# Optimization experiments

Measured on AMD Instinct MI355X. Metric: run time of the kernel, lower is better.

The kernel has to match this reference:

```python
import jax, jax.numpy as jnp
import numpy as np

PH, PW = 7, 7  # pooled_height, pooled_width
B, H, W, C, R = 4, 64, 64, 256, 128


def setup_inputs() -> dict:
    key = jax.random.key(0)
    k1, k2, k3 = jax.random.split(key, 3)
    feature_map = jax.random.normal(k1, (B, H, W, C), dtype=jnp.float32)
    # ROIs: (y_min, x_min, y_max, x_max) relative coords; sized so every
    # region has >= PH rows / PW cols (avoids empty-bin -inf edge case).
    start = jax.random.uniform(k2, (B, R, 2), minval=0.0, maxval=0.4)
    extent = jax.random.uniform(k3, (B, R, 2), minval=0.3, maxval=0.55)
    rois = jnp.concatenate([start, start + extent], axis=-1).astype(jnp.float32)
    return {"feature_map": feature_map, "rois": rois}


def _pool_image(fm, rois_img):
    # fm: (H, W, C); rois_img: (R, 4)
    h, w, _ = fm.shape
    # tf.cast(float->int32) truncates; coords are non-negative so == floor
    h0 = jnp.floor(h * rois_img[:, 0]).astype(jnp.int32)
    w0 = jnp.floor(w * rois_img[:, 1]).astype(jnp.int32)
    h1 = jnp.floor(h * rois_img[:, 2]).astype(jnp.int32)
    w1 = jnp.floor(w * rois_img[:, 3]).astype(jnp.int32)
    rh, rw = h1 - h0, w1 - w0
    hstep = jnp.maximum(rh // PH, 1)  # guard: assumes region >= pooled grid
    wstep = jnp.maximum(rw // PW, 1)

    # Map each absolute row/col to its pooled bin (or PH/PW = "outside").
    rel_h = jnp.arange(h)[None, :] - h0[:, None]            # (R, H)
    bin_h = jnp.clip(rel_h // hstep[:, None], 0, PH - 1)     # last bin extends to region end
    row_id = jnp.where((rel_h >= 0) & (rel_h < rh[:, None]), bin_h, PH)
    rel_w = jnp.arange(w)[None, :] - w0[:, None]            # (R, W)
    bin_w = jnp.clip(rel_w // wstep[:, None], 0, PW - 1)
    col_id = jnp.where((rel_w >= 0) & (rel_w < rw[:, None]), bin_w, PW)

    # Stage 1: segment-max over rows -> (R, PH, W, C)
    seg_rows = jax.vmap(
        lambda ids: jax.ops.segment_max(fm, ids, num_segments=PH + 1)
    )(row_id)[:, :PH]

    # Stage 2: segment-max over cols -> (R, PH, PW, C)
    def col_pool(t, ids):  # t: (PH, W, C)
        tt = jnp.swapaxes(t, 0, 1)  # (W, PH, C)
        s = jax.ops.segment_max(tt, ids, num_segments=PW + 1)[:PW]
        return jnp.swapaxes(s, 0, 1)  # (PH, PW, C)

    return jax.vmap(col_pool)(seg_rows, col_id)


def reference(feature_map, rois):
    # (B, R, PH, PW, C)
    return jax.vmap(_pool_image)(feature_map, rois)
```

## Files before the change

### kernel.cpp

```cpp
#include <hip/hip_runtime.h>
#include <math.h>

#define PH 7
#define PW 7
#define BB 4
#define HH 64
#define WW 64
#define CC 256
#define RR 128
#define CH4 (CC / 4)
#define BINS_PER_IMG (RR * PH * PW)
#define NBINS (BB * BINS_PER_IMG)
#define NBLK (NBINS / 4)
#define BLK_PER_IMG (NBLK / 8)
#define DEPTH 16

typedef float f4 __attribute__((ext_vector_type(4)));

__device__ __forceinline__ f4 max4(f4 a, f4 b) {
    f4 r;
    r.x = fmaxf(a.x, b.x); r.y = fmaxf(a.y, b.y);
    r.z = fmaxf(a.z, b.z); r.w = fmaxf(a.w, b.w);
    return r;
}

__device__ __forceinline__ int rfl(int x) {
    return __builtin_amdgcn_readfirstlane(x);
}

__global__ __launch_bounds__(256, 4) void ROIPoolingLayer_62079457296467_kernel(
    const float* __restrict__ fm, const float* __restrict__ rois,
    float* __restrict__ out)
{
    const int lane = threadIdx.x & 63;
    const int wave = rfl(threadIdx.x >> 6);

    const int bid   = blockIdx.x;
    const int xcd   = bid & 7;
    const int slot  = bid >> 3;
    const int b     = xcd >> 1;
    const int blkin = (xcd & 1) * BLK_PER_IMG + slot;
    const int local = blkin * 4 + wave;
    const int r     = local / (PH * PW);
    const int bin   = local - r * (PH * PW);
    const int ph    = bin / PW;
    const int pw    = bin - ph * PW;
    const int br    = b * RR + r;

    const f4 roi = ((const f4*)rois)[br];
    const int h0 = rfl((int)floorf((float)HH * roi.x));
    const int w0 = rfl((int)floorf((float)WW * roi.y));
    const int h1 = rfl((int)floorf((float)HH * roi.z));
    const int w1 = rfl((int)floorf((float)WW * roi.w));
    const int rh = h1 - h0;
    const int rw = w1 - w0;
    const int hstep = max(rh / PH, 1);
    const int wstep = max(rw / PW, 1);

    int hs = h0 + ph * hstep;
    int he = (ph == PH - 1) ? (h0 + rh) : (hs + hstep);
    he = min(he, h0 + rh);  he = min(he, HH);
    int ws = w0 + pw * wstep;
    int we = (pw == PW - 1) ? (w0 + rw) : (ws + wstep);
    we = min(we, w0 + rw);  we = min(we, WW);

    const int hbin = he - hs;
    const int wbin = we - ws;
    const int npix = hbin * wbin;

    const f4* __restrict__ fmb =
        (const f4*)fm + ((size_t)b * HH + hs) * (WW * CH4) + (size_t)ws * CH4 + lane;

    f4 acc = (f4){-INFINITY, -INFINITY, -INFINITY, -INFINITY};

    if (npix > 0) {
        const unsigned m = (65536u + (unsigned)wbin - 1) / (unsigned)wbin;
        for (int p = 0; p < npix; p += DEPTH) {
            f4 v[DEPTH];
#pragma unroll
            for (int k = 0; k < DEPTH; ++k) {
                const int pk  = min(p + k, npix - 1);
                const int q   = (int)(((unsigned)pk * m) >> 16);
                const int w   = pk - q * wbin;
                const int off = rfl(q * WW + w);
                v[k] = fmb[(size_t)off * CH4];
            }
#pragma unroll
            for (int k = 0; k < DEPTH / 2; ++k) v[k] = max4(v[k], v[k + DEPTH / 2]);
#pragma unroll
            for (int k = 0; k < DEPTH / 4; ++k) v[k] = max4(v[k], v[k + DEPTH / 4]);
#pragma unroll
            for (int k = 0; k < DEPTH / 8; ++k) v[k] = max4(v[k], v[k + DEPTH / 8]);
            acc = max4(acc, max4(v[0], v[1]));
        }
    }

    const size_t gbin = (size_t)b * BINS_PER_IMG + local;
    __builtin_nontemporal_store(acc, (f4*)out + gbin * CH4 + lane);
}

extern "C" void kernel_launch(void* const* d_in, const int* in_sizes, int n_in,
                              void* d_out, int out_size, void* d_ws, size_t ws_size,
                              hipStream_t stream) {
    const float* fm   = (const float*)d_in[0];
    const float* rois = (const float*)d_in[1];
    float* out        = (float*)d_out;
    ROIPoolingLayer_62079457296467_kernel<<<NBLK, 256, 0, stream>>>(fm, rois, out);
}
```

Measured before the change: 89.96 us.

## Process multiple bins per wave with persistent-style loop and raise occupancy

Shrinks the grid from one bin per wave to 2048 blocks, with each wave looping over up to four bins strided across the image. The load batch depth drops from 16 to 8 and launch bounds rise to 8 blocks per CU, trading per-wave memory parallelism for more resident waves and less block launch overhead. Per-bin pointer setup is hoisted out of the loop. This risks load imbalance, since bin sizes vary and each wave now handles its bins one after another.

Result: slower. 91.97 us (+2.2%).

```diff
diff --git a/kernel.cpp b/kernel.cpp
--- a/kernel.cpp
+++ b/kernel.cpp
@@ -11,9 +11,9 @@
 #define CH4 (CC / 4)
 #define BINS_PER_IMG (RR * PH * PW)
 #define NBINS (BB * BINS_PER_IMG)
-#define NBLK (NBINS / 4)
-#define BLK_PER_IMG (NBLK / 8)
-#define DEPTH 16
+#define NBLK 2048
+#define BLK_HALF 256
+#define WPI 2048
 
 typedef float f4 __attribute__((ext_vector_type(4)));
 
@@ -23,80 +23,74 @@
     r.z = fmaxf(a.z, b.z); r.w = fmaxf(a.w, b.w);
     return r;
 }
+__device__ __forceinline__ int rfl(int x) { return __builtin_amdgcn_readfirstlane(x); }
 
-__device__ __forceinline__ int rfl(int x) {
-    return __builtin_amdgcn_readfirstlane(x);
-}
-
-__global__ __launch_bounds__(256, 4) void ROIPoolingLayer_62079457296467_kernel(
+__global__ __launch_bounds__(256, 8) void ROIPoolingLayer_62079457296467_kernel(
     const float* __restrict__ fm, const float* __restrict__ rois,
     float* __restrict__ out)
 {
     const int lane = threadIdx.x & 63;
-    const int wave = rfl(threadIdx.x >> 6);
+    const int wave = rfl((int)threadIdx.x >> 6);
 
     const int bid   = blockIdx.x;
     const int xcd   = bid & 7;
-    const int slot  = bid >> 3;
     const int b     = xcd >> 1;
-    const int blkin = (xcd & 1) * BLK_PER_IMG + slot;
-    const int local = blkin * 4 + wave;
-    const int r     = local / (PH * PW);
-    const int bin   = local - r * (PH * PW);
-    const int ph    = bin / PW;
-    const int pw    = bin - ph * PW;
-    const int br    = b * RR + r;
+    const int blkin = (xcd & 1) * BLK_HALF + (bid >> 3);
+    const int wv    = blkin * 4 + wave;
 
-    const f4 roi = ((const f4*)rois)[br];
-    const int h0 = rfl((int)floorf((float)HH * roi.x));
-    const int w0 = rfl((int)floorf((float)WW * roi.y));
-    const int h1 = rfl((int)floorf((float)HH * roi.z));
-    const int w1 = rfl((int)floorf((float)WW * roi.w));
-    const int rh = h1 - h0;
-    const int rw = w1 - w0;
-    const int hstep = max(rh / PH, 1);
-    const int wstep = max(rw / PW, 1);
+    const f4* __restrict__ fmb  = (const f4*)fm + (size_t)b * (HH * WW) * CH4 + lane;
+    const f4* __restrict__ roib = (const f4*)rois + (size_t)b * RR;
+    f4* __restrict__ outb = (f4*)out + (size_t)b * BINS_PER_IMG * CH4 + lane;
 
-    int hs = h0 + ph * hstep;
-    int he = (ph == PH - 1) ? (h0 + rh) : (hs + hstep);
-    he = min(he, h0 + rh);  he = min(he, HH);
-    int ws = w0 + pw * wstep;
-    int we = (pw == PW - 1) ? (w0 + rw) : (ws + wstep);
-    we = min(we, w0 + rw);  we = min(we, WW);
+#pragma unroll
+    for (int t = 0; t < 4; ++t) {
+        const int local = wv + t * WPI;
+        if (local < BINS_PER_IMG) {
+            const int r   = local / (PH * PW);
+            const int bin = local - r * (PH * PW);
+            const int ph  = bin / PW;
+            const int pw  = bin - ph * PW;
 
-    const int hbin = he - hs;
-    const int wbin = we - ws;
-    const int npix = hbin * wbin;
+            const f4 roi = roib[r];
+            const int h0 = rfl((int)floorf((float)HH * roi.x));
+            const int w0 = rfl((int)floorf((float)WW * roi.y));
+            const int h1 = rfl((int)floorf((float)HH * roi.z));
+            const int w1 = rfl((int)floorf((float)WW * roi.w));
+            const int rh = h1 - h0, rw = w1 - w0;
+            const int hstep = max(rh / PH, 1), wstep = max(rw / PW, 1);
 
-    const f4* __restrict__ fmb =
-        (const f4*)fm + ((size_t)b * HH + hs) * (WW * CH4) + (size_t)ws * CH4 + lane;
+            int hs = h0 + ph * hstep;
+            int he = (ph == PH - 1) ? (h0 + rh) : (hs + hstep);
+            he = min(he, h0 + rh);  he = min(he, HH);
+            int ws = w0 + pw * wstep;
+            int we = (pw == PW - 1) ? (w0 + rw) : (ws + wstep);
+            we = min(we, w0 + rw);  we = min(we, WW);
 
-    f4 acc = (f4){-INFINITY, -INFINITY, -INFINITY, -INFINITY};
+            const int wbin = we - ws;
+            const int npix = (he - hs) * wbin;
+            f4 acc = (f4){-INFINITY, -INFINITY, -INFINITY, -INFINITY};
 
-    if (npix > 0) {
-        const unsigned m = (65536u + (unsigned)wbin - 1) / (unsigned)wbin;
-        for (int p = 0; p < npix; p += DEPTH) {
-            f4 v[DEPTH];
+            if (npix > 0) {
+                const int sbase = rfl(hs * WW + ws);
+                const unsigned m = (65536u + (unsigned)wbin - 1) / (unsigned)wbin;
+                for (int p = 0; p < npix; p += 8) {
+                    f4 v[8];
 #pragma unroll
-            for (int k = 0; k < DEPTH; ++k) {
-                const int pk  = min(p + k, npix - 1);
-                const int q   = (int)(((unsigned)pk * m) >> 16);
-                const int w   = pk - q * wbin;
-                const int off = rfl(q * WW + w);
-                v[k] = fmb[(size_t)off * CH4];
+                    for (int k = 0; k < 8; ++k) {
+                        const int pk  = min(p + k, npix - 1);
+                        const int q   = (int)(((unsigned)pk * m) >> 16);
+                        const int off = rfl(sbase + q * WW + (pk - q * wbin));
+                        v[k] = fmb[(size_t)off * CH4];
+                    }
+#pragma unroll
+                    for (int k = 0; k < 4; ++k) v[k] = max4(v[k], v[k + 4]);
+                    acc = max4(acc, max4(max4(v[0], v[1]), max4(v[2], v[3])));
+                }
             }
-#pragma unroll
-            for (int k = 0; k < DEPTH / 2; ++k) v[k] = max4(v[k], v[k + DEPTH / 2]);
-#pragma unroll
-            for (int k = 0; k < DEPTH / 4; ++k) v[k] = max4(v[k], v[k + DEPTH / 4]);
-#pragma unroll
-            for (int k = 0; k < DEPTH / 8; ++k) v[k] = max4(v[k], v[k + DEPTH / 8]);
-            acc = max4(acc, max4(v[0], v[1]));
+
+            __builtin_nontemporal_store(acc, outb + (size_t)local * CH4);
         }
     }
-
-    const size_t gbin = (size_t)b * BINS_PER_IMG + local;
-    __builtin_nontemporal_store(acc, (f4*)out + gbin * CH4 + lane);
 }
 
 extern "C" void kernel_launch(void* const* d_in, const int* in_sizes, int n_in,
```
